# Optimization experiments

Measured on AMD Instinct MI355X. Metric: run time of the kernel, lower is better.

## Reference

```python
import jax, jax.numpy as jnp
import numpy as np

NUM_GRAPHS = 8192
LN_EPS = 1e-5


def mlp3_ln(h, W1, b1, W2, b2, W3, b3, g, be):
    # Lin -> ReLU -> Lin -> ReLU -> Lin -> LayerNorm
    h = jax.nn.relu(h @ W1 + b1)
    h = jax.nn.relu(h @ W2 + b2)
    h = h @ W3 + b3
    mu = jnp.mean(h, axis=-1, keepdims=True)
    var = jnp.var(h, axis=-1, keepdims=True)
    return (h - mu) / jnp.sqrt(var + LN_EPS) * g + be


def setup_inputs() -> dict:
    N = 500_000
    DIN, H, DL, DG, PRE, L = 10, 20, 20, 20, 20, 20
    rng = np.random.default_rng(0)
    f = lambda *s: jnp.asarray(rng.normal(0.0, 0.1, s).astype(np.float32))
    inp = {
        'x': f(N, DIN),
        'batch': jnp.sort(jnp.asarray(rng.integers(0, NUM_GRAPHS, N).astype(np.int32))),
        # node-init MLP
        'ni_W1': f(DIN, H), 'ni_b1': f(H), 'ni_W2': f(H, H), 'ni_b2': f(H),
        'ni_W3': f(H, DL), 'ni_b3': f(DL), 'ni_g': jnp.ones(DL), 'ni_be': jnp.zeros(DL),
        # NodeModel mlp, stacked over L meta-layers
        'nm_W1': f(L, DL + DG, H), 'nm_b1': f(L, H), 'nm_W2': f(L, H, H), 'nm_b2': f(L, H),
        'nm_W3': f(L, H, DL), 'nm_b3': f(L, DL), 'nm_g': jnp.ones((L, DL)), 'nm_be': jnp.zeros((L, DL)),
        # GlobalModel mlp_pre_aggr, stacked
        'gp_W1': f(L, DL + DG, H), 'gp_b1': f(L, H), 'gp_W2': f(L, H, H), 'gp_b2': f(L, H),
        'gp_W3': f(L, H, PRE), 'gp_b3': f(L, PRE), 'gp_g': jnp.ones((L, PRE)), 'gp_be': jnp.zeros((L, PRE)),
        # GlobalModel mlp_post_aggr, stacked
        'gq_W1': f(L, PRE + DG, H), 'gq_b1': f(L, H), 'gq_W2': f(L, H, H), 'gq_b2': f(L, H),
        'gq_W3': f(L, H, DG), 'gq_b3': f(L, DG), 'gq_g': jnp.ones((L, DG)), 'gq_be': jnp.zeros((L, DG)),
    }
    return inp


def reference(x, batch, ni_W1, ni_b1, ni_W2, ni_b2, ni_W3, ni_b3, ni_g, ni_be,
              nm_W1, nm_b1, nm_W2, nm_b2, nm_W3, nm_b3, nm_g, nm_be,
              gp_W1, gp_b1, gp_W2, gp_b2, gp_W3, gp_b3, gp_g, gp_be,
              gq_W1, gq_b1, gq_W2, gq_b2, gq_W3, gq_b3, gq_g, gq_be):
    dg = gq_W3.shape[-1]
    x = mlp3_ln(x, ni_W1, ni_b1, ni_W2, ni_b2, ni_W3, ni_b3, ni_g, ni_be)
    u = jnp.zeros((NUM_GRAPHS, dg), dtype=x.dtype)

    def step(carry, p):
        x, u = carry
        (nW1, nb1, nW2, nb2, nW3, nb3, ng, nbe,
         pW1, pb1, pW2, pb2, pW3, pb3, pg, pbe,
         qW1, qb1, qW2, qb2, qW3, qb3, qg, qbe) = p
        # NodeModel: gather u per node, MLP, residual
        x = mlp3_ln(jnp.concatenate([x, u[batch]], axis=-1),
                    nW1, nb1, nW2, nb2, nW3, nb3, ng, nbe) + x
        # GlobalModel: gather, pre-aggr MLP, scatter_add, post-aggr MLP, residual
        pre = mlp3_ln(jnp.concatenate([x, u[batch]], axis=-1),
                      pW1, pb1, pW2, pb2, pW3, pb3, pg, pbe)
        agg = jax.ops.segment_sum(pre, batch, num_segments=NUM_GRAPHS)
        u = mlp3_ln(jnp.concatenate([agg, u], axis=-1),
                    qW1, qb1, qW2, qb2, qW3, qb3, qg, qbe) + u
        return (x, u), None

    ps = (nm_W1, nm_b1, nm_W2, nm_b2, nm_W3, nm_b3, nm_g, nm_be,
          gp_W1, gp_b1, gp_W2, gp_b2, gp_W3, gp_b3, gp_g, gp_be,
          gq_W1, gq_b1, gq_W2, gq_b2, gq_W3, gq_b3, gq_g, gq_be)
    (x, u), _ = jax.lax.scan(step, (x, u), ps)
    return x, u
```

## Files before the change

### kernel.cpp

```cpp
#include <hip/hip_runtime.h>

#define NG 8192
#define LN_EPS 1e-5f

typedef float v2f __attribute__((ext_vector_type(2)));


__device__ __forceinline__ float wscan_add(float x) {
  x += __int_as_float(__builtin_amdgcn_update_dpp(0, __float_as_int(x), 0x111, 0xF, 0xF, true));
  x += __int_as_float(__builtin_amdgcn_update_dpp(0, __float_as_int(x), 0x112, 0xF, 0xF, true));
  x += __int_as_float(__builtin_amdgcn_update_dpp(0, __float_as_int(x), 0x114, 0xF, 0xF, true));
  x += __int_as_float(__builtin_amdgcn_update_dpp(0, __float_as_int(x), 0x118, 0xF, 0xF, true));
  x += __int_as_float(__builtin_amdgcn_update_dpp(0, __float_as_int(x), 0x142, 0xA, 0xF, false));
  x += __int_as_float(__builtin_amdgcn_update_dpp(0, __float_as_int(x), 0x143, 0xC, 0xF, false));
  return x;
}

__device__ __forceinline__ int wscan_max(int x) {
  int t;
  t = __builtin_amdgcn_update_dpp(0, x, 0x111, 0xF, 0xF, true); x = max(x, t);
  t = __builtin_amdgcn_update_dpp(0, x, 0x112, 0xF, 0xF, true); x = max(x, t);
  t = __builtin_amdgcn_update_dpp(0, x, 0x114, 0xF, 0xF, true); x = max(x, t);
  t = __builtin_amdgcn_update_dpp(0, x, 0x118, 0xF, 0xF, true); x = max(x, t);
  t = __builtin_amdgcn_update_dpp(0, x, 0x142, 0xA, 0xF, false); x = max(x, t);
  t = __builtin_amdgcn_update_dpp(0, x, 0x143, 0xC, 0xF, false); x = max(x, t);
  return x;
}


__device__ __forceinline__ void stage4(float* dst, const float* __restrict__ src,
                                       int n4, int tid, int nt) {
  float4* d = (float4*)dst;
  const float4* s = (const float4*)src;
  for (int t = tid; t < n4; t += nt) d[t] = s[t];
}

__device__ __forceinline__ void load20v(const float* __restrict__ p, v2f v[10]) {
  const float4* q = (const float4*)p;
#pragma unroll
  for (int t = 0; t < 5; t++) {
    float4 f = q[t];
    v[2*t]   = (v2f){f.x, f.y};
    v[2*t+1] = (v2f){f.z, f.w};
  }
}

__device__ __forceinline__ void store20v(float* __restrict__ p, const v2f v[10]) {
  float4* q = (float4*)p;
#pragma unroll
  for (int t = 0; t < 5; t++)
    q[t] = make_float4(v[2*t].x, v[2*t].y, v[2*t+1].x, v[2*t+1].y);
}

__device__ __forceinline__ float elem(const v2f* a, int k) { return a[k >> 1][k & 1]; }

__device__ __forceinline__ void mlp23_ln1(
    const float* __restrict__ W2, const float* __restrict__ b2,
    const float* __restrict__ W3, const float* __restrict__ b3,
    const float* __restrict__ g,  const float* __restrict__ be,
    const v2f h1[10], v2f out[10]) {
  const v2f* W2v = (const v2f*)W2; const v2f* b2v = (const v2f*)b2;
  const v2f* W3v = (const v2f*)W3; const v2f* b3v = (const v2f*)b3;
  const v2f* gv  = (const v2f*)g;  const v2f* bev = (const v2f*)be;
  v2f h2[10];
#pragma unroll
  for (int j = 0; j < 10; j++) h2[j] = b2v[j];
#pragma unroll
  for (int k = 0; k < 20; k++) {
    float a = fmaxf(elem(h1, k), 0.0f); v2f av = {a, a};
#pragma unroll
    for (int j = 0; j < 10; j++) h2[j] += av * W2v[k*10 + j];
  }
  v2f h3[10];
#pragma unroll
  for (int j = 0; j < 10; j++) h3[j] = b3v[j];
#pragma unroll
  for (int k = 0; k < 20; k++) {
    float a = fmaxf(elem(h2, k), 0.0f); v2f av = {a, a};
#pragma unroll
    for (int j = 0; j < 10; j++) h3[j] += av * W3v[k*10 + j];
  }
  float mu = 0.0f;
#pragma unroll
  for (int j = 0; j < 10; j++) mu += h3[j].x + h3[j].y;
  mu *= 0.05f;
  float var = 0.0f;
#pragma unroll
  for (int j = 0; j < 10; j++) {
    float dx = h3[j].x - mu, dy = h3[j].y - mu;
    var += dx*dx + dy*dy;
  }
  var *= 0.05f;
  float rs = rsqrtf(var + LN_EPS);
  v2f muv = {mu, mu}, rsv = {rs, rs};
#pragma unroll
  for (int j = 0; j < 10; j++) out[j] = (h3[j] - muv) * rsv * gv[j] + bev[j];
}


__global__ __launch_bounds__(256) void k_prelayer(
    float* __restrict__ u, float* __restrict__ part, float* __restrict__ gu,
    const float* __restrict__ nmb1, const float* __restrict__ gpb1) {
  int t = blockIdx.x * 256 + threadIdx.x;
  part[t] = 0.0f;
  if (t < NG * 40) {
    int j = t % 40;
    gu[t] = (j < 20) ? nmb1[j] : gpb1[j - 20];
  }
  if (t < NG * 20) u[t] = 0.0f;
}

__global__ __launch_bounds__(256) void k_init(
    const float* __restrict__ xin, float* __restrict__ xs,
    const float* __restrict__ W1, const float* __restrict__ b1,
    const float* __restrict__ W2, const float* __restrict__ b2,
    const float* __restrict__ W3, const float* __restrict__ b3,
    const float* __restrict__ gw, const float* __restrict__ bw, int n) {
  int i = blockIdx.x * 256 + threadIdx.x;
  if (i >= n) return;
  float xi[10];
  const float2* xp = (const float2*)(xin + (size_t)i * 10);
#pragma unroll
  for (int t = 0; t < 5; t++) { float2 f = xp[t]; xi[t*2] = f.x; xi[t*2+1] = f.y; }
  const v2f* W1v = (const v2f*)W1; const v2f* b1v = (const v2f*)b1;
  v2f h1[10];
#pragma unroll
  for (int j = 0; j < 10; j++) h1[j] = b1v[j];
#pragma unroll
  for (int k = 0; k < 10; k++) {
    float a = xi[k]; v2f av = {a, a};
#pragma unroll
    for (int j = 0; j < 10; j++) h1[j] += av * W1v[k*10 + j];
  }
  v2f out[10];
  mlp23_ln1(W2, b2, W3, b3, gw, bw, h1, out);
  store20v(xs + (size_t)i * 20, out);
}

__global__ __launch_bounds__(256) void k_node(
    const int* __restrict__ batch, float* __restrict__ xs,
    const float* __restrict__ gu, float* __restrict__ part,
    const float* __restrict__ nmW1, const float* __restrict__ nmW2,
    const float* __restrict__ nmW3, const float* __restrict__ nmb2,
    const float* __restrict__ nmb3, const float* __restrict__ nmg,
    const float* __restrict__ nmbe,
    const float* __restrict__ gpW1, const float* __restrict__ gpW2,
    const float* __restrict__ gpW3, const float* __restrict__ gpb2,
    const float* __restrict__ gpb3, const float* __restrict__ gpg,
    const float* __restrict__ gpbe, int n) {
  __shared__ float sm[1280];
  int tid = threadIdx.x;
  stage4(sm + 0,    gpW1, 100, tid, 256);
  stage4(sm + 400,  gpW2, 100, tid, 256);
  stage4(sm + 800,  gpW3, 100, tid, 256);
  stage4(sm + 1200, gpb2, 5,   tid, 256);
  stage4(sm + 1220, gpb3, 5,   tid, 256);
  stage4(sm + 1240, gpg,  5,   tid, 256);
  stage4(sm + 1260, gpbe, 5,   tid, 256);
  __syncthreads();

  int i = blockIdx.x * 256 + tid;
  int lane = tid & 63;
  bool valid = i < n;
  int ic = valid ? i : (n - 1);
  int b = batch[ic];

  v2f x[10];
  load20v(xs + (size_t)ic * 20, x);

  v2f h1[10];
  load20v(gu + (size_t)b * 40, h1);
  const v2f* W1v = (const v2f*)nmW1;
#pragma unroll
  for (int k = 0; k < 20; k++) {
    float a = elem(x, k); v2f av = {a, a};
#pragma unroll
    for (int j = 0; j < 10; j++) h1[j] += av * W1v[k*10 + j];
  }
  v2f xn[10];
  mlp23_ln1(nmW2, nmb2, nmW3, nmb3, nmg, nmbe, h1, xn);
#pragma unroll
  for (int j = 0; j < 10; j++) xn[j] += x[j];
  if (valid) store20v(xs + (size_t)ic * 20, xn);

  v2f p1[10];
  load20v(gu + (size_t)b * 40 + 20, p1);
  const v2f* G1v = (const v2f*)sm;
#pragma unroll
  for (int k = 0; k < 20; k++) {
    float a = elem(xn, k); v2f av = {a, a};
#pragma unroll
    for (int j = 0; j < 10; j++) p1[j] += av * G1v[k*10 + j];
  }
  v2f pre[10];
  mlp23_ln1(sm + 400, sm + 1200, sm + 800, sm + 1220, sm + 1240, sm + 1260,
            p1, pre);

  int key = valid ? b : -1;
  if (!valid) {
#pragma unroll
    for (int j = 0; j < 10; j++) pre[j] = (v2f){0.0f, 0.0f};
  }
  int pk = __builtin_amdgcn_update_dpp(-1, key, 0x138, 0xF, 0xF, false);
  int nk = __builtin_amdgcn_update_dpp(-2, key, 0x130, 0xF, 0xF, false);
  bool isstart = (key != pk);
  int st = wscan_max(isstart ? lane : 0);

#pragma unroll
  for (int j = 0; j < 10; j++) {
    pre[j].x = wscan_add(pre[j].x);
    pre[j].y = wscan_add(pre[j].y);
  }

  int pl = (st > 0) ? (st - 1) : 0;
  float use = (st > 0) ? 1.0f : 0.0f;
  v2f fl[10];
#pragma unroll
  for (int j = 0; j < 10; j++) {
    float bx = __shfl(pre[j].x, pl);
    float by = __shfl(pre[j].y, pl);
    fl[j].x = pre[j].x - use * bx;
    fl[j].y = pre[j].y - use * by;
  }
  bool runend = valid && (nk != key);
  if (runend) {
    int slot = (i >> 6) & 3;
    float* pp = part + (size_t)b * 80 + slot * 20;
#pragma unroll
    for (int j = 0; j < 10; j++) {
      pp[2*j]     = fl[j].x;
      pp[2*j + 1] = fl[j].y;
    }
  }
}

__global__ __launch_bounds__(64) void k_global(
    float* __restrict__ u, float* __restrict__ part, float* __restrict__ gu,
    const float* __restrict__ qW1, const float* __restrict__ qb1,
    const float* __restrict__ qW2, const float* __restrict__ qb2,
    const float* __restrict__ qW3, const float* __restrict__ qb3,
    const float* __restrict__ qg,  const float* __restrict__ qbe,
    const float* __restrict__ nmW1u, const float* __restrict__ nmb1n,
    const float* __restrict__ gpW1u, const float* __restrict__ gpb1n,
    int has_next) {
  int g = blockIdx.x * 64 + threadIdx.x;
  float* pg = part + (size_t)g * 80;
  v2f s0[10], s1[10], s2[10], s3[10];
  load20v(pg,      s0);
  load20v(pg + 20, s1);
  load20v(pg + 40, s2);
  load20v(pg + 60, s3);
  v2f a[10];
#pragma unroll
  for (int j = 0; j < 10; j++) a[j] = ((s0[j] + s1[j]) + s2[j]) + s3[j];

  v2f uu[10];
  load20v(u + (size_t)g * 20, uu);
  const v2f* qW1v = (const v2f*)qW1; const v2f* qb1v = (const v2f*)qb1;
  v2f h1[10];
#pragma unroll
  for (int j = 0; j < 10; j++) h1[j] = qb1v[j];
#pragma unroll
  for (int k = 0; k < 20; k++) {
    float v = elem(a, k); v2f av = {v, v};
#pragma unroll
    for (int j = 0; j < 10; j++) h1[j] += av * qW1v[k*10 + j];
  }
#pragma unroll
  for (int k = 0; k < 20; k++) {
    float v = elem(uu, k); v2f av = {v, v};
#pragma unroll
    for (int j = 0; j < 10; j++) h1[j] += av * qW1v[200 + k*10 + j];
  }
  v2f un[10];
  mlp23_ln1(qW2, qb2, qW3, qb3, qg, qbe, h1, un);
#pragma unroll
  for (int j = 0; j < 10; j++) un[j] += uu[j];
  store20v(u + (size_t)g * 20, un);

  v2f z[10];
#pragma unroll
  for (int j = 0; j < 10; j++) z[j] = (v2f){0.0f, 0.0f};
  store20v(pg,      z);
  store20v(pg + 20, z);
  store20v(pg + 40, z);
  store20v(pg + 60, z);

  if (has_next) {
    const v2f* nW = (const v2f*)nmW1u; const v2f* nb = (const v2f*)nmb1n;
    const v2f* gW = (const v2f*)gpW1u; const v2f* gb = (const v2f*)gpb1n;
    v2f gn[10], gg2[10];
#pragma unroll
    for (int j = 0; j < 10; j++) { gn[j] = nb[j]; gg2[j] = gb[j]; }
#pragma unroll
    for (int k = 0; k < 20; k++) {
      float v = elem(un, k); v2f av = {v, v};
#pragma unroll
      for (int j = 0; j < 10; j++) {
        gn[j]  += av * nW[k*10 + j];
        gg2[j] += av * gW[k*10 + j];
      }
    }
    store20v(gu + (size_t)g * 40, gn);
    store20v(gu + (size_t)g * 40 + 20, gg2);
  }
}


extern "C" void kernel_launch(void* const* d_in, const int* in_sizes, int n_in,
                              void* d_out, int out_size, void* d_ws, size_t ws_size,
                              hipStream_t stream) {
  const float* x_in  = (const float*)d_in[0];
  const int*   batch = (const int*)  d_in[1];
  const float* ni_W1 = (const float*)d_in[2];
  const float* ni_b1 = (const float*)d_in[3];
  const float* ni_W2 = (const float*)d_in[4];
  const float* ni_b2 = (const float*)d_in[5];
  const float* ni_W3 = (const float*)d_in[6];
  const float* ni_b3 = (const float*)d_in[7];
  const float* ni_g  = (const float*)d_in[8];
  const float* ni_be = (const float*)d_in[9];
  const float* nm_W1 = (const float*)d_in[10];
  const float* nm_b1 = (const float*)d_in[11];
  const float* nm_W2 = (const float*)d_in[12];
  const float* nm_b2 = (const float*)d_in[13];
  const float* nm_W3 = (const float*)d_in[14];
  const float* nm_b3 = (const float*)d_in[15];
  const float* nm_g  = (const float*)d_in[16];
  const float* nm_be = (const float*)d_in[17];
  const float* gp_W1 = (const float*)d_in[18];
  const float* gp_b1 = (const float*)d_in[19];
  const float* gp_W2 = (const float*)d_in[20];
  const float* gp_b2 = (const float*)d_in[21];
  const float* gp_W3 = (const float*)d_in[22];
  const float* gp_b3 = (const float*)d_in[23];
  const float* gp_g  = (const float*)d_in[24];
  const float* gp_be = (const float*)d_in[25];
  const float* gq_W1 = (const float*)d_in[26];
  const float* gq_b1 = (const float*)d_in[27];
  const float* gq_W2 = (const float*)d_in[28];
  const float* gq_b2 = (const float*)d_in[29];
  const float* gq_W3 = (const float*)d_in[30];
  const float* gq_b3 = (const float*)d_in[31];
  const float* gq_g  = (const float*)d_in[32];
  const float* gq_be = (const float*)d_in[33];

  const int N = in_sizes[0] / 10;
  float* xs = (float*)d_out;
  float* u  = xs + (size_t)N * 20;

  float* part = (float*)d_ws;
  float* gu   = part + NG * 80;

  const int L = 20;
  const int nblk = (N + 255) / 256;

  k_prelayer<<<(NG * 80) / 256, 256, 0, stream>>>(u, part, gu, nm_b1, gp_b1);
  k_init<<<nblk, 256, 0, stream>>>(x_in, xs, ni_W1, ni_b1, ni_W2, ni_b2,
                                   ni_W3, ni_b3, ni_g, ni_be, N);
  for (int l = 0; l < L; l++) {
    k_node<<<nblk, 256, 0, stream>>>(batch, xs, gu, part,
        nm_W1 + (size_t)l * 800, nm_W2 + (size_t)l * 400, nm_W3 + (size_t)l * 400,
        nm_b2 + l * 20, nm_b3 + l * 20, nm_g + l * 20, nm_be + l * 20,
        gp_W1 + (size_t)l * 800, gp_W2 + (size_t)l * 400, gp_W3 + (size_t)l * 400,
        gp_b2 + l * 20, gp_b3 + l * 20, gp_g + l * 20, gp_be + l * 20, N);
    int has_next = (l < L - 1);
    k_global<<<NG / 64, 64, 0, stream>>>(u, part, gu,
        gq_W1 + (size_t)l * 800, gq_b1 + l * 20,
        gq_W2 + (size_t)l * 400, gq_b2 + l * 20,
        gq_W3 + (size_t)l * 400, gq_b3 + l * 20,
        gq_g + l * 20, gq_be + l * 20,
        nm_W1 + (size_t)(l + 1) * 800 + 400, nm_b1 + (l + 1) * 20,
        gp_W1 + (size_t)(l + 1) * 800 + 400, gp_b1 + (l + 1) * 20,
        has_next);
  }
}
```

Baseline: 1.532 ms.

## Process two nodes per thread in k_node with pairwise segmented scan

k_node now handles two consecutive nodes per thread, sharing each weight load across both nodes' MLP evaluations. The segmented wave-level reduction is rewritten to combine each pair locally, scan over 128-node spans, and handle run boundaries inside pairs. Launch bounds add a minimum-occupancy hint. The partial-slot index changes to match the larger per-wave span. Costs are double register pressure per thread and more complex scan logic, with half as many threads for latency hiding.

Measured after the change: 1.922 ms. +25.4%, slower.

```diff
diff --git a/kernel.cpp b/kernel.cpp
--- a/kernel.cpp
+++ b/kernel.cpp
@@ -27,6 +27,10 @@
   return x;
 }
 
+__device__ __forceinline__ float dpp_prev(float x) {
+  return __int_as_float(__builtin_amdgcn_update_dpp(0, __float_as_int(x), 0x138, 0xF, 0xF, false));
+}
+
 
 __device__ __forceinline__ void stage4(float* dst, const float* __restrict__ src,
                                        int n4, int tid, int nt) {
@@ -53,6 +57,25 @@
 }
 
 __device__ __forceinline__ float elem(const v2f* a, int k) { return a[k >> 1][k & 1]; }
+
+__device__ __forceinline__ void ln10(const v2f h3[10], const v2f* gv, const v2f* bev,
+                                     v2f out[10]) {
+  float mu = 0.0f;
+#pragma unroll
+  for (int j = 0; j < 10; j++) mu += h3[j].x + h3[j].y;
+  mu *= 0.05f;
+  float var = 0.0f;
+#pragma unroll
+  for (int j = 0; j < 10; j++) {
+    float dx = h3[j].x - mu, dy = h3[j].y - mu;
+    var += dx*dx + dy*dy;
+  }
+  var *= 0.05f;
+  float rs = rsqrtf(var + LN_EPS);
+  v2f muv = {mu, mu}, rsv = {rs, rs};
+#pragma unroll
+  for (int j = 0; j < 10; j++) out[j] = (h3[j] - muv) * rsv * gv[j] + bev[j];
+}
 
 __device__ __forceinline__ void mlp23_ln1(
     const float* __restrict__ W2, const float* __restrict__ b2,
@@ -80,21 +103,45 @@
 #pragma unroll
     for (int j = 0; j < 10; j++) h3[j] += av * W3v[k*10 + j];
   }
-  float mu = 0.0f;
-#pragma unroll
-  for (int j = 0; j < 10; j++) mu += h3[j].x + h3[j].y;
-  mu *= 0.05f;
-  float var = 0.0f;
-#pragma unroll
-  for (int j = 0; j < 10; j++) {
-    float dx = h3[j].x - mu, dy = h3[j].y - mu;
-    var += dx*dx + dy*dy;
-  }
-  var *= 0.05f;
-  float rs = rsqrtf(var + LN_EPS);
-  v2f muv = {mu, mu}, rsv = {rs, rs};
-#pragma unroll
-  for (int j = 0; j < 10; j++) out[j] = (h3[j] - muv) * rsv * gv[j] + bev[j];
+  ln10(h3, gv, bev, out);
+}
+
+__device__ __forceinline__ void mlp23_ln1_x2(
+    const float* __restrict__ W2, const float* __restrict__ b2,
+    const float* __restrict__ W3, const float* __restrict__ b3,
+    const float* __restrict__ g,  const float* __restrict__ be,
+    const v2f h1a[10], const v2f h1b[10], v2f outa[10], v2f outb[10]) {
+  const v2f* W2v = (const v2f*)W2; const v2f* b2v = (const v2f*)b2;
+  const v2f* W3v = (const v2f*)W3; const v2f* b3v = (const v2f*)b3;
+  const v2f* gv  = (const v2f*)g;  const v2f* bev = (const v2f*)be;
+  v2f h2a[10], h2b[10];
+#pragma unroll
+  for (int j = 0; j < 10; j++) { h2a[j] = b2v[j]; h2b[j] = b2v[j]; }
+#pragma unroll
+  for (int k = 0; k < 20; k++) {
+    float a0 = fmaxf(elem(h1a, k), 0.0f), a1 = fmaxf(elem(h1b, k), 0.0f);
+    v2f av0 = {a0, a0}, av1 = {a1, a1};
+#pragma unroll
+    for (int j = 0; j < 10; j++) {
+      v2f w = W2v[k*10 + j];
+      h2a[j] += av0 * w; h2b[j] += av1 * w;
+    }
+  }
+  v2f h3a[10], h3b[10];
+#pragma unroll
+  for (int j = 0; j < 10; j++) { h3a[j] = b3v[j]; h3b[j] = b3v[j]; }
+#pragma unroll
+  for (int k = 0; k < 20; k++) {
+    float a0 = fmaxf(elem(h2a, k), 0.0f), a1 = fmaxf(elem(h2b, k), 0.0f);
+    v2f av0 = {a0, a0}, av1 = {a1, a1};
+#pragma unroll
+    for (int j = 0; j < 10; j++) {
+      v2f w = W3v[k*10 + j];
+      h3a[j] += av0 * w; h3b[j] += av1 * w;
+    }
+  }
+  ln10(h3a, gv, bev, outa);
+  ln10(h3b, gv, bev, outb);
 }
 
 
@@ -137,7 +184,7 @@
   store20v(xs + (size_t)i * 20, out);
 }
 
-__global__ __launch_bounds__(256) void k_node(
+__global__ __launch_bounds__(256, 4) void k_node(
     const int* __restrict__ batch, float* __restrict__ xs,
     const float* __restrict__ gu, float* __restrict__ part,
     const float* __restrict__ nmW1, const float* __restrict__ nmW2,
@@ -159,77 +206,133 @@
   stage4(sm + 1260, gpbe, 5,   tid, 256);
   __syncthreads();
 
-  int i = blockIdx.x * 256 + tid;
+  int t = blockIdx.x * 256 + tid;
   int lane = tid & 63;
-  bool valid = i < n;
-  int ic = valid ? i : (n - 1);
-  int b = batch[ic];
-
-  v2f x[10];
-  load20v(xs + (size_t)ic * 20, x);
-
-  v2f h1[10];
-  load20v(gu + (size_t)b * 40, h1);
-  const v2f* W1v = (const v2f*)nmW1;
-#pragma unroll
-  for (int k = 0; k < 20; k++) {
-    float a = elem(x, k); v2f av = {a, a};
-#pragma unroll
-    for (int j = 0; j < 10; j++) h1[j] += av * W1v[k*10 + j];
-  }
-  v2f xn[10];
-  mlp23_ln1(nmW2, nmb2, nmW3, nmb3, nmg, nmbe, h1, xn);
-#pragma unroll
-  for (int j = 0; j < 10; j++) xn[j] += x[j];
-  if (valid) store20v(xs + (size_t)ic * 20, xn);
-
-  v2f p1[10];
-  load20v(gu + (size_t)b * 40 + 20, p1);
+  int i0 = t * 2, i1 = t * 2 + 1;
+  bool valid0 = i0 < n, valid1 = i1 < n;
+  int ic0 = valid0 ? i0 : (n - 1);
+  int ic1 = valid1 ? i1 : (n - 1);
+  int b0 = batch[ic0];
+  int b1 = batch[ic1];
+
+  v2f h1a[10], h1b[10];
+  load20v(gu + (size_t)b0 * 40, h1a);
+  load20v(gu + (size_t)b1 * 40, h1b);
+  {
+    v2f x0[10], x1[10];
+    load20v(xs + (size_t)ic0 * 20, x0);
+    load20v(xs + (size_t)ic1 * 20, x1);
+    const v2f* W1v = (const v2f*)nmW1;
+#pragma unroll
+    for (int k = 0; k < 20; k++) {
+      float a0 = elem(x0, k), a1 = elem(x1, k);
+      v2f av0 = {a0, a0}, av1 = {a1, a1};
+#pragma unroll
+      for (int j = 0; j < 10; j++) {
+        v2f w = W1v[k*10 + j];
+        h1a[j] += av0 * w; h1b[j] += av1 * w;
+      }
+    }
+  }
+  v2f xa[10], xb[10];
+  mlp23_ln1_x2(nmW2, nmb2, nmW3, nmb3, nmg, nmbe, h1a, h1b, xa, xb);
+  {
+    v2f x0[10], x1[10];
+    load20v(xs + (size_t)ic0 * 20, x0);
+    load20v(xs + (size_t)ic1 * 20, x1);
+#pragma unroll
+    for (int j = 0; j < 10; j++) { xa[j] += x0[j]; xb[j] += x1[j]; }
+  }
+  if (valid0) store20v(xs + (size_t)ic0 * 20, xa);
+  if (valid1) store20v(xs + (size_t)ic1 * 20, xb);
+
+  v2f p1a[10], p1b[10];
+  load20v(gu + (size_t)b0 * 40 + 20, p1a);
+  load20v(gu + (size_t)b1 * 40 + 20, p1b);
   const v2f* G1v = (const v2f*)sm;
 #pragma unroll
   for (int k = 0; k < 20; k++) {
-    float a = elem(xn, k); v2f av = {a, a};
-#pragma unroll
-    for (int j = 0; j < 10; j++) p1[j] += av * G1v[k*10 + j];
-  }
-  v2f pre[10];
-  mlp23_ln1(sm + 400, sm + 1200, sm + 800, sm + 1220, sm + 1240, sm + 1260,
-            p1, pre);
-
-  int key = valid ? b : -1;
-  if (!valid) {
-#pragma unroll
-    for (int j = 0; j < 10; j++) pre[j] = (v2f){0.0f, 0.0f};
-  }
-  int pk = __builtin_amdgcn_update_dpp(-1, key, 0x138, 0xF, 0xF, false);
-  int nk = __builtin_amdgcn_update_dpp(-2, key, 0x130, 0xF, 0xF, false);
-  bool isstart = (key != pk);
-  int st = wscan_max(isstart ? lane : 0);
-
+    float a0 = elem(xa, k), a1 = elem(xb, k);
+    v2f av0 = {a0, a0}, av1 = {a1, a1};
+#pragma unroll
+    for (int j = 0; j < 10; j++) {
+      v2f w = G1v[k*10 + j];
+      p1a[j] += av0 * w; p1b[j] += av1 * w;
+    }
+  }
+  v2f pre0[10], pre1[10];
+  mlp23_ln1_x2(sm + 400, sm + 1200, sm + 800, sm + 1220, sm + 1240, sm + 1260,
+               p1a, p1b, pre0, pre1);
+
+  int k0 = valid0 ? b0 : -1;
+  int k1 = valid1 ? b1 : -1;
+  if (!valid0) {
+#pragma unroll
+    for (int j = 0; j < 10; j++) pre0[j] = (v2f){0.0f, 0.0f};
+  }
+  if (!valid1) {
+#pragma unroll
+    for (int j = 0; j < 10; j++) pre1[j] = (v2f){0.0f, 0.0f};
+  }
+
+  int pk1 = __builtin_amdgcn_update_dpp(-1, k1, 0x138, 0xF, 0xF, false);
+  int nk0 = __builtin_amdgcn_update_dpp(-2, k0, 0x130, 0xF, 0xF, false);
+  bool samepair = (k0 == k1);
+
+  v2f pv[10];
+  float sp = samepair ? 1.0f : 0.0f;
 #pragma unroll
   for (int j = 0; j < 10; j++) {
-    pre[j].x = wscan_add(pre[j].x);
-    pre[j].y = wscan_add(pre[j].y);
-  }
+    pv[j].x = pre1[j].x + sp * pre0[j].x;
+    pv[j].y = pre1[j].y + sp * pre0[j].y;
+  }
+  bool head = (!samepair) || (k0 != pk1);
+  int st = wscan_max(head ? lane : 0);
+
+#pragma unroll
+  for (int j = 0; j < 10; j++) {
+    pv[j].x = wscan_add(pv[j].x);
+    pv[j].y = wscan_add(pv[j].y);
+  }
+
+  int slot = (i0 >> 7) & 3;
 
   int pl = (st > 0) ? (st - 1) : 0;
   float use = (st > 0) ? 1.0f : 0.0f;
-  v2f fl[10];
+  bool runend1 = valid1 && (k1 != nk0);
+  bool chain0 = (pk1 == k0);
+  int pst = __shfl(st, (lane - 1) & 63);
+  float useP = chain0 ? 1.0f : 0.0f;
+  float useB = (chain0 && pst > 0) ? 1.0f : 0.0f;
+  int blidx = (pst > 0) ? (pst - 1) : 0;
+  bool runend0 = valid0 && (k0 != k1);
+
+  v2f R1[10], R0[10];
 #pragma unroll
   for (int j = 0; j < 10; j++) {
-    float bx = __shfl(pre[j].x, pl);
-    float by = __shfl(pre[j].y, pl);
-    fl[j].x = pre[j].x - use * bx;
-    fl[j].y = pre[j].y - use * by;
-  }
-  bool runend = valid && (nk != key);
-  if (runend) {
-    int slot = (i >> 6) & 3;
-    float* pp = part + (size_t)b * 80 + slot * 20;
+    float sx = pv[j].x, sy = pv[j].y;
+    R1[j].x = sx - use * __shfl(sx, pl);
+    R1[j].y = sy - use * __shfl(sy, pl);
+    float spx = dpp_prev(sx), spy = dpp_prev(sy);
+    float bx = __shfl(sx, blidx), by = __shfl(sy, blidx);
+    R0[j].x = pre0[j].x + useP * spx - useB * bx;
+    R0[j].y = pre0[j].y + useP * spy - useB * by;
+  }
+
+  if (runend1) {
+    float* pp = part + (size_t)k1 * 80 + slot * 20;
 #pragma unroll
     for (int j = 0; j < 10; j++) {
-      pp[2*j]     = fl[j].x;
-      pp[2*j + 1] = fl[j].y;
+      pp[2*j]     = R1[j].x;
+      pp[2*j + 1] = R1[j].y;
+    }
+  }
+  if (runend0) {
+    float* pp = part + (size_t)k0 * 80 + slot * 20;
+#pragma unroll
+    for (int j = 0; j < 10; j++) {
+      pp[2*j]     = R0[j].x;
+      pp[2*j + 1] = R0[j].y;
     }
   }
 }
@@ -245,14 +348,17 @@
     int has_next) {
   int g = blockIdx.x * 64 + threadIdx.x;
   float* pg = part + (size_t)g * 80;
-  v2f s0[10], s1[10], s2[10], s3[10];
-  load20v(pg,      s0);
-  load20v(pg + 20, s1);
-  load20v(pg + 40, s2);
-  load20v(pg + 60, s3);
-  v2f a[10];
-#pragma unroll
-  for (int j = 0; j < 10; j++) a[j] = ((s0[j] + s1[j]) + s2[j]) + s3[j];
+  v2f a[10], tmp[10];
+  load20v(pg, a);
+  load20v(pg + 20, tmp);
+#pragma unroll
+  for (int j = 0; j < 10; j++) a[j] += tmp[j];
+  load20v(pg + 40, tmp);
+#pragma unroll
+  for (int j = 0; j < 10; j++) a[j] += tmp[j];
+  load20v(pg + 60, tmp);
+#pragma unroll
+  for (int j = 0; j < 10; j++) a[j] += tmp[j];
 
   v2f uu[10];
   load20v(u + (size_t)g * 20, uu);
@@ -353,13 +459,15 @@
   float* gu   = part + NG * 80;
 
   const int L = 20;
-  const int nblk = (N + 255) / 256;
+  const int nblk  = (N + 255) / 256;
+  const int nhalf = (N + 1) / 2;
+  const int nblk2 = (nhalf + 255) / 256;
 
   k_prelayer<<<(NG * 80) / 256, 256, 0, stream>>>(u, part, gu, nm_b1, gp_b1);
   k_init<<<nblk, 256, 0, stream>>>(x_in, xs, ni_W1, ni_b1, ni_W2, ni_b2,
                                    ni_W3, ni_b3, ni_g, ni_be, N);
   for (int l = 0; l < L; l++) {
-    k_node<<<nblk, 256, 0, stream>>>(batch, xs, gu, part,
+    k_node<<<nblk2, 256, 0, stream>>>(batch, xs, gu, part,
         nm_W1 + (size_t)l * 800, nm_W2 + (size_t)l * 400, nm_W3 + (size_t)l * 400,
         nm_b2 + l * 20, nm_b3 + l * 20, nm_g + l * 20, nm_be + l * 20,
         gp_W1 + (size_t)l * 800, gp_W2 + (size_t)l * 400, gp_W3 + (size_t)l * 400,
```

## Split per-graph global MLP across four lanes with LDS-staged transposed weights

Applied to the files above, without the earlier changes.

The global-update kernel now assigns four threads per graph instead of one. Each lane reduces one partial slot, and the four slots are combined with xor shuffles. Each lane computes 5 of the 20 outputs per layer from weights staged, transposed, in shared memory, then broadcasts activations within its group of four via shuffles. The aim is more parallelism (only 8192 threads before) and lower per-thread register pressure in this small launch, at the cost of shuffle traffic and per-block weight staging.

New measurement: 1.333 ms. -13.0%, faster.

```diff
diff --git a/kernel.cpp b/kernel.cpp
--- a/kernel.cpp
+++ b/kernel.cpp
@@ -234,7 +234,7 @@
   }
 }
 
-__global__ __launch_bounds__(64) void k_global(
+__global__ __launch_bounds__(128) void k_global(
     float* __restrict__ u, float* __restrict__ part, float* __restrict__ gu,
     const float* __restrict__ qW1, const float* __restrict__ qb1,
     const float* __restrict__ qW2, const float* __restrict__ qb2,
@@ -243,66 +243,160 @@
     const float* __restrict__ nmW1u, const float* __restrict__ nmb1n,
     const float* __restrict__ gpW1u, const float* __restrict__ gpb1n,
     int has_next) {
-  int g = blockIdx.x * 64 + threadIdx.x;
-  float* pg = part + (size_t)g * 80;
-  v2f s0[10], s1[10], s2[10], s3[10];
-  load20v(pg,      s0);
-  load20v(pg + 20, s1);
-  load20v(pg + 40, s2);
-  load20v(pg + 60, s3);
-  v2f a[10];
-#pragma unroll
-  for (int j = 0; j < 10; j++) a[j] = ((s0[j] + s1[j]) + s2[j]) + s3[j];
-
-  v2f uu[10];
-  load20v(u + (size_t)g * 20, uu);
-  const v2f* qW1v = (const v2f*)qW1; const v2f* qb1v = (const v2f*)qb1;
-  v2f h1[10];
-#pragma unroll
-  for (int j = 0; j < 10; j++) h1[j] = qb1v[j];
-#pragma unroll
-  for (int k = 0; k < 20; k++) {
-    float v = elem(a, k); v2f av = {v, v};
-#pragma unroll
-    for (int j = 0; j < 10; j++) h1[j] += av * qW1v[k*10 + j];
-  }
-#pragma unroll
-  for (int k = 0; k < 20; k++) {
-    float v = elem(uu, k); v2f av = {v, v};
-#pragma unroll
-    for (int j = 0; j < 10; j++) h1[j] += av * qW1v[200 + k*10 + j];
-  }
-  v2f un[10];
-  mlp23_ln1(qW2, qb2, qW3, qb3, qg, qbe, h1, un);
-#pragma unroll
-  for (int j = 0; j < 10; j++) un[j] += uu[j];
-  store20v(u + (size_t)g * 20, un);
-
-  v2f z[10];
-#pragma unroll
-  for (int j = 0; j < 10; j++) z[j] = (v2f){0.0f, 0.0f};
-  store20v(pg,      z);
-  store20v(pg + 20, z);
-  store20v(pg + 40, z);
-  store20v(pg + 60, z);
+  __shared__ float sW1T[20 * 40];
+  __shared__ float sW2T[20 * 20];
+  __shared__ float sW3T[20 * 20];
+  __shared__ float sNT[20 * 20];
+  __shared__ float sGT[20 * 20];
+  __shared__ float sB[140];
+  int tid = threadIdx.x;
+  for (int e = tid; e < 800; e += 128) sW1T[(e % 20) * 40 + (e / 20)] = qW1[e];
+  for (int e = tid; e < 400; e += 128) {
+    int k = e / 20, j = e % 20;
+    sW2T[j * 20 + k] = qW2[e];
+    sW3T[j * 20 + k] = qW3[e];
+    sNT[j * 20 + k]  = nmW1u[e];
+    sGT[j * 20 + k]  = gpW1u[e];
+  }
+  if (tid < 20) {
+    sB[tid]       = qb1[tid];
+    sB[20 + tid]  = qb2[tid];
+    sB[40 + tid]  = qb3[tid];
+    sB[60 + tid]  = qg[tid];
+    sB[80 + tid]  = qbe[tid];
+    sB[100 + tid] = nmb1n[tid];
+    sB[120 + tid] = gpb1n[tid];
+  }
+  __syncthreads();
+
+  int t = blockIdx.x * 128 + tid;
+  int g = t >> 2;
+  int q = t & 3;
+  int lane = tid & 63;
+  int gl = lane & ~3;
+
+  float a[20];
+  {
+    const float4* p = (const float4*)(part + (size_t)g * 80 + q * 20);
+#pragma unroll
+    for (int i = 0; i < 5; i++) {
+      float4 f = p[i];
+      a[4*i] = f.x; a[4*i+1] = f.y; a[4*i+2] = f.z; a[4*i+3] = f.w;
+    }
+  }
+#pragma unroll
+  for (int i = 0; i < 20; i++) {
+    a[i] += __shfl_xor(a[i], 1);
+    a[i] += __shfl_xor(a[i], 2);
+  }
+
+  float uu[20];
+  {
+    const float4* p = (const float4*)(u + (size_t)g * 20);
+#pragma unroll
+    for (int i = 0; i < 5; i++) {
+      float4 f = p[i];
+      uu[4*i] = f.x; uu[4*i+1] = f.y; uu[4*i+2] = f.z; uu[4*i+3] = f.w;
+    }
+  }
+
+  float h1[5];
+#pragma unroll
+  for (int o = 0; o < 5; o++) {
+    int j = q * 5 + o;
+    const v2f* w = (const v2f*)(sW1T + j * 40);
+    v2f acc = {0.0f, 0.0f};
+#pragma unroll
+    for (int kk = 0; kk < 10; kk++) acc += (v2f){a[2*kk], a[2*kk+1]} * w[kk];
+#pragma unroll
+    for (int kk = 0; kk < 10; kk++) acc += (v2f){uu[2*kk], uu[2*kk+1]} * w[10 + kk];
+    h1[o] = sB[j] + acc.x + acc.y;
+  }
+
+  float r1[20];
+#pragma unroll
+  for (int k = 0; k < 20; k++)
+    r1[k] = fmaxf(__shfl(h1[k % 5], gl + (k / 5)), 0.0f);
+
+  float h2[5];
+#pragma unroll
+  for (int o = 0; o < 5; o++) {
+    int j = q * 5 + o;
+    const v2f* w = (const v2f*)(sW2T + j * 20);
+    v2f acc = {0.0f, 0.0f};
+#pragma unroll
+    for (int kk = 0; kk < 10; kk++) acc += (v2f){r1[2*kk], r1[2*kk+1]} * w[kk];
+    h2[o] = sB[20 + j] + acc.x + acc.y;
+  }
+
+  float r2[20];
+#pragma unroll
+  for (int k = 0; k < 20; k++)
+    r2[k] = fmaxf(__shfl(h2[k % 5], gl + (k / 5)), 0.0f);
+
+  float h3[5];
+#pragma unroll
+  for (int o = 0; o < 5; o++) {
+    int j = q * 5 + o;
+    const v2f* w = (const v2f*)(sW3T + j * 20);
+    v2f acc = {0.0f, 0.0f};
+#pragma unroll
+    for (int kk = 0; kk < 10; kk++) acc += (v2f){r2[2*kk], r2[2*kk+1]} * w[kk];
+    h3[o] = sB[40 + j] + acc.x + acc.y;
+  }
+
+  float s = h3[0] + h3[1] + h3[2] + h3[3] + h3[4];
+  s += __shfl_xor(s, 1);
+  s += __shfl_xor(s, 2);
+  float mu = s * 0.05f;
+  float d = 0.0f;
+#pragma unroll
+  for (int o = 0; o < 5; o++) { float dd = h3[o] - mu; d += dd * dd; }
+  d += __shfl_xor(d, 1);
+  d += __shfl_xor(d, 2);
+  float rs = rsqrtf(d * 0.05f + LN_EPS);
+
+  float un[5];
+#pragma unroll
+  for (int o = 0; o < 5; o++) {
+    int j = q * 5 + o;
+    un[o] = (h3[o] - mu) * rs * sB[60 + j] + sB[80 + j] + uu[j];
+  }
+#pragma unroll
+  for (int o = 0; o < 5; o++) u[(size_t)g * 20 + q * 5 + o] = un[o];
+
+  {
+    float4* p = (float4*)(part + (size_t)g * 80 + q * 20);
+#pragma unroll
+    for (int i = 0; i < 5; i++) p[i] = make_float4(0.f, 0.f, 0.f, 0.f);
+  }
 
   if (has_next) {
-    const v2f* nW = (const v2f*)nmW1u; const v2f* nb = (const v2f*)nmb1n;
-    const v2f* gW = (const v2f*)gpW1u; const v2f* gb = (const v2f*)gpb1n;
-    v2f gn[10], gg2[10];
-#pragma unroll
-    for (int j = 0; j < 10; j++) { gn[j] = nb[j]; gg2[j] = gb[j]; }
-#pragma unroll
-    for (int k = 0; k < 20; k++) {
-      float v = elem(un, k); v2f av = {v, v};
-#pragma unroll
-      for (int j = 0; j < 10; j++) {
-        gn[j]  += av * nW[k*10 + j];
-        gg2[j] += av * gW[k*10 + j];
+    float ru[20];
+#pragma unroll
+    for (int k = 0; k < 20; k++)
+      ru[k] = __shfl(un[k % 5], gl + (k / 5));
+    float gn[5], gg[5];
+#pragma unroll
+    for (int o = 0; o < 5; o++) {
+      int j = q * 5 + o;
+      const v2f* wn = (const v2f*)(sNT + j * 20);
+      const v2f* wg = (const v2f*)(sGT + j * 20);
+      v2f an = {0.0f, 0.0f}, ag = {0.0f, 0.0f};
+#pragma unroll
+      for (int kk = 0; kk < 10; kk++) {
+        v2f rv = {ru[2*kk], ru[2*kk+1]};
+        an += rv * wn[kk];
+        ag += rv * wg[kk];
       }
+      gn[o] = sB[100 + j] + an.x + an.y;
+      gg[o] = sB[120 + j] + ag.x + ag.y;
     }
-    store20v(gu + (size_t)g * 40, gn);
-    store20v(gu + (size_t)g * 40 + 20, gg2);
+#pragma unroll
+    for (int o = 0; o < 5; o++) {
+      gu[(size_t)g * 40 + q * 5 + o]      = gn[o];
+      gu[(size_t)g * 40 + 20 + q * 5 + o] = gg[o];
+    }
   }
 }
 
@@ -365,7 +459,7 @@
         gp_W1 + (size_t)l * 800, gp_W2 + (size_t)l * 400, gp_W3 + (size_t)l * 400,
         gp_b2 + l * 20, gp_b3 + l * 20, gp_g + l * 20, gp_be + l * 20, N);
     int has_next = (l < L - 1);
-    k_global<<<NG / 64, 64, 0, stream>>>(u, part, gu,
+    k_global<<<(NG * 4) / 128, 128, 0, stream>>>(u, part, gu,
         gq_W1 + (size_t)l * 800, gq_b1 + l * 20,
         gq_W2 + (size_t)l * 400, gq_b2 + l * 20,
         gq_W3 + (size_t)l * 400, gq_b3 + l * 20,
```
